# Kernel optimization log

Measured on AMD Instinct MI355X. Metric: run time of the kernel, lower is better.

The kernel has to match this reference:

```python
import jax, jax.numpy as jnp
import numpy as np

B, H, W = 4, 512, 512
N_PER_BATCH = 65536
N = B * N_PER_BATCH
C_IN, C_OUT = 64, 64
BN_EPS = 1e-3


def _build_rulebook():
    """Random active sites on a BxHxW grid; neighbor_idx[n,k] = row of k-th 3x3
    neighbor of active site n, or -1 if that cell is inactive / out of bounds."""
    rng = np.random.default_rng(0)
    grid = -np.ones((B, H + 2, W + 2), np.int32)  # padded coord->row lookup
    ys_all, xs_all = [], []
    for b in range(B):
        flat = rng.choice(H * W, size=N_PER_BATCH, replace=False)
        ys, xs = (flat // W).astype(np.int64), (flat % W).astype(np.int64)
        grid[b, ys + 1, xs + 1] = np.arange(b * N_PER_BATCH, (b + 1) * N_PER_BATCH, dtype=np.int32)
        ys_all.append(ys); xs_all.append(xs)
    neighbor = np.empty((N, 9), np.int32)
    offsets = [(dy, dx) for dy in (-1, 0, 1) for dx in (-1, 0, 1)]
    for b in range(B):
        ys, xs = ys_all[b], xs_all[b]
        sl = slice(b * N_PER_BATCH, (b + 1) * N_PER_BATCH)
        for k, (dy, dx) in enumerate(offsets):
            neighbor[sl, k] = grid[b, ys + 1 + dy, xs + 1 + dx]
    return neighbor


def setup_inputs() -> dict:
    key = jax.random.key(0)
    k1, k2, k3, k4, k5 = jax.random.split(key, 5)
    return {
        "features": jax.random.normal(k1, (N, C_IN), jnp.float32),
        "weight": jax.random.normal(k2, (9, C_IN, C_OUT), jnp.float32) * 0.05,
        "bias": jax.random.normal(k3, (C_OUT,), jnp.float32) * 0.05,
        "gamma": jax.random.uniform(k4, (C_OUT,), jnp.float32, 0.5, 1.5),
        "beta": jax.random.normal(k5, (C_OUT,), jnp.float32) * 0.05,
        "neighbor_idx": jnp.asarray(_build_rulebook()),
    }


def reference(features, weight, bias, gamma, beta, neighbor_idx):
    # Submanifold sparse 3x3 conv: out[n] = bias + sum_k feat[nbr(n,k)] @ W[k]
    n = features.shape[0]
    out = jnp.broadcast_to(bias, (n, bias.shape[0]))
    for k in range(9):  # fixed kernel taps
        idx = neighbor_idx[:, k]
        valid = idx >= 0
        g = jnp.where(valid[:, None], features[jnp.where(valid, idx, 0)], 0.0)
        out = out + g @ weight[k]
    # BatchNorm1d (training mode) over the active-point axis, eps=1e-3
    mean = jnp.mean(out, axis=0)
    var = jnp.mean(jnp.square(out - mean), axis=0)  # biased variance
    out_bn = (out - mean) * jax.lax.rsqrt(var + BN_EPS) * gamma + beta
    return out, out_bn
```

## Files before the change

### kernel.cpp

```cpp
#include <hip/hip_runtime.h>
#include <hip/hip_bf16.h>

#define N_TOTAL 262144
#define BN_EPS  1e-3f

typedef float f32x4  __attribute__((ext_vector_type(4)));
typedef short bf16x8 __attribute__((ext_vector_type(8)));

typedef __attribute__((address_space(1))) const unsigned int as1cu;
typedef __attribute__((address_space(3))) unsigned int       as3u;

#define SCALE_F   4096
#define WFRAG_OFF 17408
#define FEATB_OFF 131072
#define FEAT_BLOCKS 16384
#define WPACK_BLOCKS 144

template<bool DO_FEAT>
__global__ void prepare_kernel(const float* __restrict__ feat,
                               unsigned short* __restrict__ featb_region,
                               const float* __restrict__ W,
                               unsigned short* __restrict__ wfrag,
                               float* __restrict__ gstats)
{
    const int b = blockIdx.x;
    if (b < FEAT_BLOCKS) {
        if (DO_FEAT) {
            const size_t i = (size_t)b * 256 + threadIdx.x;
            const float4 v = ((const float4*)feat)[i];
            union { __hip_bfloat162 h[2]; uint2 u; } p;
            p.h[0] = __float22bfloat162_rn(make_float2(v.x, v.y));
            p.h[1] = __float22bfloat162_rn(make_float2(v.z, v.w));
            ((uint2*)(featb_region + 64))[i] = p.u;
        }
    } else if (b < FEAT_BLOCKS + WPACK_BLOCKS) {
        const int e = (b - FEAT_BLOCKS) * 256 + threadIdx.x;
        const int f  = e >> 9;
        const int r  = e & 511;
        const int L  = r >> 3;
        const int j  = r & 7;
        const int nb = f & 3;
        const int kk = (f >> 2) & 1;
        const int k9 = f >> 3;
        const int kci = kk * 32 + ((L >> 4) << 3) + j;
        const int n   = nb * 16 + (L & 15);
        __hip_bfloat16 bb = __float2bfloat16(W[k9 * 4096 + kci * 64 + n]);
        wfrag[e] = *reinterpret_cast<unsigned short*>(&bb);
    } else {
        for (int i = threadIdx.x; i < 4096; i += 256) gstats[i] = 0.f;
        if (threadIdx.x < 64) featb_region[threadIdx.x] = 0;
    }
}

__global__ __launch_bounds__(256, 3)
void conv_mfma_kernel(const unsigned short* __restrict__ featb,
                      const unsigned short* __restrict__ wfrag,
                      const float* __restrict__ bias,
                      const int*   __restrict__ nb9,
                      float* __restrict__ out,
                      float* __restrict__ gstats)
{
    __shared__ int IL[128 * 9];
    __shared__ __align__(16) unsigned short Abuf[3 * 4 * 2 * 2 * 512];

    const int tid  = threadIdx.x;
    const int lane = tid & 63;
    const int wave = tid >> 6;
    const int quad = lane >> 4;
    const int l16  = lane & 15;
    const int rowbase = wave * 32;

    for (int i = tid; i < 128 * 9; i += 256)
        IL[i] = nb9[(size_t)blockIdx.x * 1152 + i];
    __syncthreads();

    int ofs[9][2];
#pragma unroll
    for (int t = 0; t < 9; ++t)
#pragma unroll
        for (int mb = 0; mb < 2; ++mb) {
            const int id = IL[(rowbase + mb * 16 + l16) * 9 + t];
            ofs[t][mb] = (id < 0) ? -64 : (id << 6);
        }

    f32x4 acc[2][4];
#pragma unroll
    for (int mb = 0; mb < 2; ++mb)
#pragma unroll
        for (int nb = 0; nb < 4; ++nb)
            acc[mb][nb] = (f32x4){0.f, 0.f, 0.f, 0.f};

    bf16x8 Bf[2][8];

    auto loadBtap = [&](int t) {
#pragma unroll
        for (int f = 0; f < 8; ++f)
            Bf[t & 1][f] = *(const bf16x8*)(wfrag + (t * 8 + f) * 512 + lane * 8);
    };
    auto asyncA = [&](int t) {
        const int buf = t % 3;
#pragma unroll
        for (int mb = 0; mb < 2; ++mb)
#pragma unroll
            for (int kk = 0; kk < 2; ++kk) {
                const unsigned short* g = featb + ofs[t][mb] + kk * 32 + quad * 8;
                unsigned short* l = &Abuf[(((buf * 4 + wave) * 2 + mb) * 2 + kk) * 512];
                __builtin_amdgcn_global_load_lds((as1cu*)g, (as3u*)l, 16, 0, 0);
            }
    };

    loadBtap(0);
    asyncA(0);
    asyncA(1);

#pragma unroll
    for (int t = 0; t < 9; ++t) {
        if (t + 1 < 9) loadBtap(t + 1);
        if (t + 2 < 9) asyncA(t + 2);
        if (t < 7)       asm volatile("s_waitcnt vmcnt(16)" ::: "memory");
        else if (t == 7) asm volatile("s_waitcnt vmcnt(12)" ::: "memory");
        else             asm volatile("s_waitcnt vmcnt(0)"  ::: "memory");

        const int buf = t % 3;
#pragma unroll
        for (int kk = 0; kk < 2; ++kk)
#pragma unroll
            for (int mb = 0; mb < 2; ++mb) {
                const bf16x8 a = *(const bf16x8*)
                    &Abuf[(((buf * 4 + wave) * 2 + mb) * 2 + kk) * 512 + lane * 8];
#pragma unroll
                for (int nb = 0; nb < 4; ++nb)
                    acc[mb][nb] = __builtin_amdgcn_mfma_f32_16x16x32_bf16(
                        a, Bf[t & 1][kk * 4 + nb], acc[mb][nb], 0, 0, 0);
            }
    }

    const size_t row0 = (size_t)blockIdx.x * 128 + rowbase;
    const int rep = (blockIdx.x & 31) * 128;
    float s[4], sq[4];
#pragma unroll
    for (int nb = 0; nb < 4; ++nb) { s[nb] = 0.f; sq[nb] = 0.f; }

#pragma unroll
    for (int nb = 0; nb < 4; ++nb) {
        const float b = bias[nb * 16 + l16];
#pragma unroll
        for (int mb = 0; mb < 2; ++mb) {
            const f32x4 v = acc[mb][nb];
#pragma unroll
            for (int i = 0; i < 4; ++i) {
                const float o = v[i] + b;
                out[(row0 + mb * 16 + quad * 4 + i) * 64 + nb * 16 + l16] = o;
                s[nb]  += o;
                sq[nb] += o * o;
            }
        }
    }
#pragma unroll
    for (int nb = 0; nb < 4; ++nb) {
        float ss = s[nb], qq = sq[nb];
        ss += __shfl_xor(ss, 16, 64);  qq += __shfl_xor(qq, 16, 64);
        ss += __shfl_xor(ss, 32, 64);  qq += __shfl_xor(qq, 32, 64);
        if (quad == 0) {
            atomicAdd(&gstats[rep + nb * 16 + l16],      ss);
            atomicAdd(&gstats[rep + 64 + nb * 16 + l16], qq);
        }
    }
}

__global__ void conv_fallback_kernel(const float* __restrict__ feat,
                                     const float* __restrict__ W,
                                     const float* __restrict__ bias,
                                     const int* __restrict__ nb9,
                                     float* __restrict__ out,
                                     float* __restrict__ gstats)
{
    const int n = blockIdx.x;
    const int c = threadIdx.x;
    float a = bias[c];
    for (int k = 0; k < 9; ++k) {
        const int id = nb9[(size_t)n * 9 + k];
        if (id >= 0) {
            const float* fr = feat + (size_t)id * 64;
            const float* wk = W + k * 4096 + c;
            for (int ci = 0; ci < 64; ++ci) a = fmaf(fr[ci], wk[ci * 64], a);
        }
    }
    out[(size_t)n * 64 + c] = a;
    atomicAdd(&gstats[(n & 31) * 128 + c], a);
    atomicAdd(&gstats[(n & 31) * 128 + 64 + c], a * a);
}

__global__ void zero_stats_kernel(float* __restrict__ gstats)
{
    for (int i = threadIdx.x + blockIdx.x * 256; i < 4096; i += 256 * 16)
        gstats[i] = 0.f;
}

__global__ void bn_stats_kernel(const float* __restrict__ gamma,
                                const float* __restrict__ beta,
                                float* __restrict__ gs)
{
    const int c = threadIdx.x;
    float s = 0.f, q = 0.f;
#pragma unroll
    for (int r = 0; r < 32; ++r) { s += gs[r * 128 + c]; q += gs[r * 128 + 64 + c]; }
    const float inv_n = 1.f / (float)N_TOTAL;
    const float mean  = s * inv_n;
    const float var   = q * inv_n - mean * mean;
    const float sc    = gamma[c] * rsqrtf(var + BN_EPS);
    gs[SCALE_F + c]      = sc;
    gs[SCALE_F + 64 + c] = beta[c] - mean * sc;
}

__global__ void bn_apply_kernel(const float* __restrict__ out,
                                const float* __restrict__ gs,
                                float* __restrict__ out_bn)
{
    const size_t i  = (size_t)blockIdx.x * blockDim.x + threadIdx.x;
    const int    c4 = ((int)i & 15) << 2;
    const float4 v  = ((const float4*)out)[i];
    const float4 sc = *(const float4*)(gs + SCALE_F + c4);
    const float4 sh = *(const float4*)(gs + SCALE_F + 64 + c4);
    float4 o;
    o.x = fmaf(v.x, sc.x, sh.x);
    o.y = fmaf(v.y, sc.y, sh.y);
    o.z = fmaf(v.z, sc.z, sh.z);
    o.w = fmaf(v.w, sc.w, sh.w);
    ((float4*)out_bn)[i] = o;
}

extern "C" void kernel_launch(void* const* d_in, const int* in_sizes, int n_in,
                              void* d_out, int out_size, void* d_ws, size_t ws_size,
                              hipStream_t stream)
{
    const float* feat  = (const float*)d_in[0];
    const float* W     = (const float*)d_in[1];
    const float* bias  = (const float*)d_in[2];
    const float* gamma = (const float*)d_in[3];
    const float* beta  = (const float*)d_in[4];
    const int*   nb9   = (const int*)  d_in[5];

    float* out    = (float*)d_out;
    float* out_bn = out + (size_t)N_TOTAL * 64;

    float*          gstats       = (float*)d_ws;
    unsigned short* wfrag        = (unsigned short*)((char*)d_ws + WFRAG_OFF);
    unsigned short* featb_region = (unsigned short*)((char*)d_ws + FEATB_OFF);

    const bool use_featb =
        ws_size >= (size_t)FEATB_OFF + 128 + (size_t)N_TOTAL * 64 * sizeof(unsigned short);

    if (use_featb) {
        prepare_kernel<true><<<FEAT_BLOCKS + WPACK_BLOCKS + 1, 256, 0, stream>>>(
            feat, featb_region, W, wfrag, gstats);
        conv_mfma_kernel<<<N_TOTAL / 128, 256, 0, stream>>>(
            featb_region + 64, wfrag, bias, nb9, out, gstats);
    } else {
        zero_stats_kernel<<<16, 256, 0, stream>>>(gstats);
        conv_fallback_kernel<<<N_TOTAL, 64, 0, stream>>>(
            feat, W, bias, nb9, out, gstats);
    }
    bn_stats_kernel<<<1, 64, 0, stream>>>(gamma, beta, gstats);
    bn_apply_kernel<<<(N_TOTAL * 64 / 4) / 256, 256, 0, stream>>>(out, gstats, out_bn);
}
```

Measured before the change: 254.8 us.

## Deepen conv prefetch pipeline, swizzle tile order, fuse BN stats into apply

The conv kernel now prefetches A tiles three taps ahead through a 4-slot LDS ring and keeps weight fragments two taps ahead in three register sets. It reuses the ring to stage the neighbor list, and lowers the launch-bounds occupancy hint from 3 to 2 blocks per CU. Block indices are swizzled so consecutive blocks handle tiles spread across the grid. The separate single-block BN stats kernel is removed: each apply block recomputes scale and shift into shared memory and then processes four float4 chunks per thread. This saves one launch but repeats the small reduction in every block, and the deeper pipeline costs more registers and LDS, which lowers occupancy.

Result: no change. 256.4 us (+0.6%).

```diff
diff --git a/kernel.cpp b/kernel.cpp
--- a/kernel.cpp
+++ b/kernel.cpp
@@ -10,7 +10,6 @@
 typedef __attribute__((address_space(1))) const unsigned int as1cu;
 typedef __attribute__((address_space(3))) unsigned int       as3u;
 
-#define SCALE_F   4096
 #define WFRAG_OFF 17408
 #define FEATB_OFF 131072
 #define FEAT_BLOCKS 16384
@@ -52,7 +51,7 @@
     }
 }
 
-__global__ __launch_bounds__(256, 3)
+__global__ __launch_bounds__(256, 2)
 void conv_mfma_kernel(const unsigned short* __restrict__ featb,
                       const unsigned short* __restrict__ wfrag,
                       const float* __restrict__ bias,
@@ -60,8 +59,8 @@
                       float* __restrict__ out,
                       float* __restrict__ gstats)
 {
-    __shared__ int IL[128 * 9];
-    __shared__ __align__(16) unsigned short Abuf[3 * 4 * 2 * 2 * 512];
+    __shared__ __align__(16) unsigned short Abuf[4 * 4 * 2 * 2 * 512];
+    int* IL = (int*)Abuf;
 
     const int tid  = threadIdx.x;
     const int lane = tid & 63;
@@ -69,9 +68,10 @@
     const int quad = lane >> 4;
     const int l16  = lane & 15;
     const int rowbase = wave * 32;
+    const int tile = ((blockIdx.x & 7) << 8) | (blockIdx.x >> 3);
 
     for (int i = tid; i < 128 * 9; i += 256)
-        IL[i] = nb9[(size_t)blockIdx.x * 1152 + i];
+        IL[i] = nb9[(size_t)tile * 1152 + i];
     __syncthreads();
 
     int ofs[9][2];
@@ -82,6 +82,7 @@
             const int id = IL[(rowbase + mb * 16 + l16) * 9 + t];
             ofs[t][mb] = (id < 0) ? -64 : (id << 6);
         }
+    __syncthreads();
 
     f32x4 acc[2][4];
 #pragma unroll
@@ -90,15 +91,15 @@
         for (int nb = 0; nb < 4; ++nb)
             acc[mb][nb] = (f32x4){0.f, 0.f, 0.f, 0.f};
 
-    bf16x8 Bf[2][8];
+    bf16x8 Bf[3][8];
 
     auto loadBtap = [&](int t) {
 #pragma unroll
         for (int f = 0; f < 8; ++f)
-            Bf[t & 1][f] = *(const bf16x8*)(wfrag + (t * 8 + f) * 512 + lane * 8);
+            Bf[t % 3][f] = *(const bf16x8*)(wfrag + (t * 8 + f) * 512 + lane * 8);
     };
     auto asyncA = [&](int t) {
-        const int buf = t % 3;
+        const int buf = t & 3;
 #pragma unroll
         for (int mb = 0; mb < 2; ++mb)
 #pragma unroll
@@ -111,17 +112,20 @@
 
     loadBtap(0);
     asyncA(0);
+    loadBtap(1);
     asyncA(1);
+    asyncA(2);
 
 #pragma unroll
     for (int t = 0; t < 9; ++t) {
-        if (t + 1 < 9) loadBtap(t + 1);
-        if (t + 2 < 9) asyncA(t + 2);
-        if (t < 7)       asm volatile("s_waitcnt vmcnt(16)" ::: "memory");
+        if (t + 2 < 9) loadBtap(t + 2);
+        if (t + 3 < 9) asyncA(t + 3);
+        if (t < 6)       asm volatile("s_waitcnt vmcnt(28)" ::: "memory");
+        else if (t == 6) asm volatile("s_waitcnt vmcnt(24)" ::: "memory");
         else if (t == 7) asm volatile("s_waitcnt vmcnt(12)" ::: "memory");
         else             asm volatile("s_waitcnt vmcnt(0)"  ::: "memory");
 
-        const int buf = t % 3;
+        const int buf = t & 3;
 #pragma unroll
         for (int kk = 0; kk < 2; ++kk)
 #pragma unroll
@@ -131,12 +135,12 @@
 #pragma unroll
                 for (int nb = 0; nb < 4; ++nb)
                     acc[mb][nb] = __builtin_amdgcn_mfma_f32_16x16x32_bf16(
-                        a, Bf[t & 1][kk * 4 + nb], acc[mb][nb], 0, 0, 0);
+                        a, Bf[t % 3][kk * 4 + nb], acc[mb][nb], 0, 0, 0);
             }
     }
 
-    const size_t row0 = (size_t)blockIdx.x * 128 + rowbase;
-    const int rep = (blockIdx.x & 31) * 128;
+    const size_t row0 = (size_t)tile * 128 + rowbase;
+    const int rep = (tile & 31) * 128;
     float s[4], sq[4];
 #pragma unroll
     for (int nb = 0; nb < 4; ++nb) { s[nb] = 0.f; sq[nb] = 0.f; }
@@ -197,37 +201,38 @@
         gstats[i] = 0.f;
 }
 
-__global__ void bn_stats_kernel(const float* __restrict__ gamma,
-                                const float* __restrict__ beta,
-                                float* __restrict__ gs)
-{
-    const int c = threadIdx.x;
-    float s = 0.f, q = 0.f;
-#pragma unroll
-    for (int r = 0; r < 32; ++r) { s += gs[r * 128 + c]; q += gs[r * 128 + 64 + c]; }
-    const float inv_n = 1.f / (float)N_TOTAL;
-    const float mean  = s * inv_n;
-    const float var   = q * inv_n - mean * mean;
-    const float sc    = gamma[c] * rsqrtf(var + BN_EPS);
-    gs[SCALE_F + c]      = sc;
-    gs[SCALE_F + 64 + c] = beta[c] - mean * sc;
-}
-
 __global__ void bn_apply_kernel(const float* __restrict__ out,
                                 const float* __restrict__ gs,
+                                const float* __restrict__ gamma,
+                                const float* __restrict__ beta,
                                 float* __restrict__ out_bn)
 {
-    const size_t i  = (size_t)blockIdx.x * blockDim.x + threadIdx.x;
-    const int    c4 = ((int)i & 15) << 2;
-    const float4 v  = ((const float4*)out)[i];
-    const float4 sc = *(const float4*)(gs + SCALE_F + c4);
-    const float4 sh = *(const float4*)(gs + SCALE_F + 64 + c4);
-    float4 o;
-    o.x = fmaf(v.x, sc.x, sh.x);
-    o.y = fmaf(v.y, sc.y, sh.y);
-    o.z = fmaf(v.z, sc.z, sh.z);
-    o.w = fmaf(v.w, sc.w, sh.w);
-    ((float4*)out_bn)[i] = o;
+    __shared__ float sc_s[64], sh_s[64];
+    const int t = threadIdx.x;
+    if (t < 64) {
+        float s = 0.f, q = 0.f;
+#pragma unroll
+        for (int r = 0; r < 32; ++r) { s += gs[r * 128 + t]; q += gs[r * 128 + 64 + t]; }
+        const float inv_n = 1.f / (float)N_TOTAL;
+        const float mean  = s * inv_n;
+        const float var   = q * inv_n - mean * mean;
+        const float sc    = gamma[t] * rsqrtf(var + BN_EPS);
+        sc_s[t] = sc;
+        sh_s[t] = beta[t] - mean * sc;
+    }
+    __syncthreads();
+#pragma unroll
+    for (int it = 0; it < 4; ++it) {
+        const size_t i  = ((size_t)blockIdx.x * 4 + it) * 256 + t;
+        const int    c4 = ((int)i & 15) << 2;
+        const float4 v  = ((const float4*)out)[i];
+        float4 o;
+        o.x = fmaf(v.x, sc_s[c4],     sh_s[c4]);
+        o.y = fmaf(v.y, sc_s[c4 + 1], sh_s[c4 + 1]);
+        o.z = fmaf(v.z, sc_s[c4 + 2], sh_s[c4 + 2]);
+        o.w = fmaf(v.w, sc_s[c4 + 3], sh_s[c4 + 3]);
+        ((float4*)out_bn)[i] = o;
+    }
 }
 
 extern "C" void kernel_launch(void* const* d_in, const int* in_sizes, int n_in,
@@ -261,6 +266,6 @@
         conv_fallback_kernel<<<N_TOTAL, 64, 0, stream>>>(
             feat, W, bias, nb9, out, gstats);
     }
-    bn_stats_kernel<<<1, 64, 0, stream>>>(gamma, beta, gstats);
-    bn_apply_kernel<<<(N_TOTAL * 64 / 4) / 256, 256, 0, stream>>>(out, gstats, out_bn);
-}
+    bn_apply_kernel<<<(N_TOTAL * 64 / 4) / (256 * 4), 256, 0, stream>>>(
+        out, gstats, gamma, beta, out_bn);
+}
```
